# Kernel tuning notes

Measured on AMD Instinct MI355X. Metric: run time of the kernel, lower is better.

The kernel has to match this reference:

```python
import jax, jax.numpy as jnp
import numpy as np

N_AGENTS = 32
N_HEADS = 8
HEAD_DIM = 32          # atten_dim // n_heads
HID = 256              # rnn_hidden_dim
ATT = 256              # atten_dim
N_ACT = 32
NEG = -1e9             # finite stand-in for -inf; exp underflows to 0 in softmax


def setup_inputs() -> dict:
    key = jax.random.key(0)
    ks = jax.random.split(key, 20)
    B, N, E = 4096, 64, 128
    w = lambda k, shape: (jax.random.normal(k, shape, jnp.float32) * 0.05)
    return {
        "inputs": jax.random.normal(ks[0], (B, N, E), jnp.float32),
        "hidden_state": jax.random.normal(ks[1], (B, N_AGENTS, HID), jnp.float32) * 0.1,
        "fc1_w": w(ks[2], (HID, E)), "fc1_b": jnp.zeros((HID,), jnp.float32),
        "q_w": w(ks[3], (ATT, HID)), "q_b": jnp.zeros((ATT,), jnp.float32),
        "k_w": w(ks[4], (ATT, HID)), "k_b": jnp.zeros((ATT,), jnp.float32),
        "v_w": w(ks[5], (ATT, HID)), "v_b": jnp.zeros((ATT,), jnp.float32),
        "w_ih": w(ks[6], (3 * HID, ATT)), "w_hh": w(ks[7], (3 * HID, HID)),
        "b_ih": jnp.zeros((3 * HID,), jnp.float32), "b_hh": jnp.zeros((3 * HID,), jnp.float32),
        "out_w": w(ks[8], (N_ACT, HID)), "out_b": jnp.zeros((N_ACT,), jnp.float32),
        "obs_mask": jax.random.randint(ks[9], (B, N, N), 0, 2).astype(bool),
        "scenario_mask": jax.random.randint(ks[10], (B, N_AGENTS), 0, 2).astype(bool),
    }


def reference(inputs, hidden_state, fc1_w, fc1_b, q_w, q_b, k_w, k_b, v_w, v_b,
              w_ih, w_hh, b_ih, b_hh, out_w, out_b, obs_mask, scenario_mask):
    B, N, _ = inputs.shape
    A, nh, e = N_AGENTS, N_HEADS, HEAD_DIM
    # fc1 + ReLU: [B, N, HID]
    x = jax.nn.relu(inputs @ fc1_w.T + fc1_b)
    # multi-head projections; queries only for the first A entities (agents)
    q = (x[:, :A] @ q_w.T + q_b).reshape(B, A, nh, e).transpose(0, 2, 1, 3)   # [B,nh,A,e]
    k = (x @ k_w.T + k_b).reshape(B, N, nh, e).transpose(0, 2, 3, 1)          # [B,nh,e,N]
    v = jax.nn.relu(x @ v_w.T + v_b).reshape(B, N, nh, e).transpose(0, 2, 1, 3)  # [B,nh,N,e]
    score = jnp.einsum('bhae,bhen->bhan', q, k) / np.float32(np.sqrt(e))      # [B,nh,A,N]
    m = obs_mask[:, :A, :][:, None, :, :]                                      # [B,1,A,N]
    score = jnp.where(m, NEG, score)
    w = jax.nn.softmax(score, axis=-1)
    # original: fully-masked rows give NaN then are zeroed; here zero all masked slots
    w = jnp.where(m, 0.0, w)
    att = jnp.einsum('bhan,bhne->bhae', w, v)                                  # [B,nh,A,e]
    att = att.transpose(0, 2, 1, 3).reshape(B * A, nh * e)                     # [B*A, ATT]
    # GRUCell step (PyTorch gate ordering: r, z, n)
    h0 = hidden_state.reshape(B * A, HID)
    gi = att @ w_ih.T + b_ih
    gh = h0 @ w_hh.T + b_hh
    ir, iz, in_ = jnp.split(gi, 3, axis=-1)
    hr, hz, hn = jnp.split(gh, 3, axis=-1)
    r = jax.nn.sigmoid(ir + hr)
    z = jax.nn.sigmoid(iz + hz)
    n = jnp.tanh(in_ + r * hn)
    h = (1.0 - z) * n + z * h0
    h = h.reshape(B, A, HID)
    am = scenario_mask[:, :, None]                                             # [B,A,1]
    h = jnp.where(am, 0.0, h)
    q_out = h @ out_w.T + out_b
    q_out = jnp.where(am, 0.0, q_out)
    return q_out, h
```

## Files before the change

### kernel.cpp

```cpp
#include <hip/hip_runtime.h>


using bfrag = __attribute__((ext_vector_type(8))) short;
using s4    = __attribute__((ext_vector_type(4))) short;
using ffrag = __attribute__((ext_vector_type(4))) float;

#define MFMA(a,b,c) __builtin_amdgcn_mfma_f32_16x16x32_bf16((a),(b),(c),0,0,0)
#define SWZ(row,col,S,xm) ((row)*(S) + ((((col)&~7) ^ (((row)&(xm))<<3)) | ((col)&7)))

#define OFF_A2   0L
#define OFF_FC1  67108864L
#define OFF_QKV  67141632L
#define OFF_W6   67338240L
#define OFF_OW   67731456L
#define OFF_FLAG 67739648L
#define WS_NEED_BYTES 135479552L

__device__ inline unsigned short f2bf(float x){
  union { float f; unsigned u; } v; v.f = x;
  unsigned r = v.u + 0x7fffu + ((v.u >> 16) & 1u);
  return (unsigned short)(r >> 16);
}
__device__ inline bool getmask(const void* p, long i, int byteflag){
  return byteflag ? (((const unsigned char*)p)[i] != 0)
                  : (((const int*)p)[i] != 0);
}
__device__ inline ffrag fzero(){ ffrag z; z[0]=0.f; z[1]=0.f; z[2]=0.f; z[3]=0.f; return z; }
__device__ inline void gload16(const short* g, short* l){
  __builtin_amdgcn_global_load_lds((const __attribute__((address_space(1))) void*)g,
                                   (__attribute__((address_space(3))) void*)l, 16, 0, 0);
}
__device__ inline bfrag packbf(const float* p){
  float4 f0 = *(const float4*)p; float4 f1 = *(const float4*)(p+4);
  bfrag v;
  v[0]=(short)f2bf(f0.x); v[1]=(short)f2bf(f0.y); v[2]=(short)f2bf(f0.z); v[3]=(short)f2bf(f0.w);
  v[4]=(short)f2bf(f1.x); v[5]=(short)f2bf(f1.y); v[6]=(short)f2bf(f1.z); v[7]=(short)f2bf(f1.w);
  return v;
}

__global__ void k0_prep(const float* __restrict__ fc1, const float* __restrict__ qw,
    const float* __restrict__ kw, const float* __restrict__ vw, const float* __restrict__ wih,
    const float* __restrict__ whh, const float* __restrict__ ow,
    const void* __restrict__ obsm, short* __restrict__ ws){
  long tid = (long)blockIdx.x*blockDim.x + threadIdx.x;
  long n = (long)gridDim.x*blockDim.x;
  if (tid == 0){
    const int* mi = (const int*)obsm;
    int f = 0;
    for (int i=0;i<256;i++){ if ((unsigned)mi[i] > 1u){ f = 1; break; } }
    ((int*)(ws + OFF_FLAG))[0] = f;
  }
  for (long i=tid; i<32768; i+=n){
    int R = (int)(i>>7), C = (int)(i&127);
    int s = R>>6, colr = R&63, ct = colr>>4, ll = colr&15;
    int ks = C>>5, rem = C&31, lh = rem>>3, j = rem&7;
    long dst = ((long)((s*4+ks)*4+ct))*512 + (lh*16+ll)*8 + j;
    ws[OFF_FC1 + dst] = (short)f2bf(fc1[i]);
  }
  for (long i=tid; i<65536; i+=n){
    int R = (int)(i>>8), C = (int)(i&255);
    int cb = R>>6, colr = R&63, ct = colr>>4, ll = colr&15;
    int ks = C>>5, rem = C&31, lh = rem>>3, j = rem&7;
    long fo = ((long)ks)*4 + ct;
    long dst = (long)(lh*16+ll)*8 + j + fo*512;
    ws[OFF_QKV + ((long)(0*4+cb))*16384 + dst] = (short)f2bf(qw[i]);
    ws[OFF_QKV + ((long)(1*4+cb))*16384 + dst] = (short)f2bf(kw[i]);
    ws[OFF_QKV + ((long)(2*4+cb))*16384 + dst] = (short)f2bf(vw[i]);
  }
  for (long i=tid; i<196608; i+=n){
    int gate = (int)(i >> 16);
    int grow = (int)((i >> 8) & 255);
    int c = (int)(i & 255);
    int jb = grow >> 5, row = grow & 31;
    int cs = c ^ ((row&7)<<3);
    ws[OFF_W6 + ((long)((jb*6 + gate)*32 + row))*256 + cs]     = (short)f2bf(wih[i]);
    ws[OFF_W6 + ((long)((jb*6 + 3 + gate)*32 + row))*256 + cs] = (short)f2bf(whh[i]);
  }
  for (long i=tid; i<8192; i+=n) ws[OFF_OW+i] = (short)f2bf(ow[i]);
}

__global__ __launch_bounds__(512) void k1_fused(const float* __restrict__ inp,
    const short* __restrict__ fc1F, const float* __restrict__ fc1_b,
    const short* __restrict__ qkvF,
    const float* __restrict__ qb, const float* __restrict__ kb, const float* __restrict__ vb,
    const void* __restrict__ obsm, short* __restrict__ A2, const int* __restrict__ flagp){
  __shared__ __align__(16) short smem[59392];
  short* x_s  = smem;
  short* a_s  = smem + 16384;
  short* q_s  = smem + 16384;
  short* k_s  = smem + 24576;
  short* vT_s = smem + 40960;
  unsigned char* m8 = (unsigned char*)(smem + 57344);
  int t = threadIdx.x; int b = blockIdx.x;
  int lane = t&63, w = t>>6, lr = lane&15, ko = lane>>4;
  int mflag = *flagp;
  #pragma unroll
  for (int i=0;i<2;i++){
    int c = t + i*512; int row = c>>4; int cc = (c&15)*8;
    *(bfrag*)(a_s + SWZ(row, cc, 128, 7)) = packbf(inp + ((long)b*64 + row)*128 + cc);
  }
  if (mflag){
    uchar4 mv = *(const uchar4*)((const unsigned char*)obsm + (long)b*4096 + t*4);
    m8[t*4]=mv.x; m8[t*4+1]=mv.y; m8[t*4+2]=mv.z; m8[t*4+3]=mv.w;
  } else {
    int4 mv = *(const int4*)((const int*)obsm + (long)b*4096 + t*4);
    m8[t*4]  =(unsigned char)(mv.x!=0); m8[t*4+1]=(unsigned char)(mv.y!=0);
    m8[t*4+2]=(unsigned char)(mv.z!=0); m8[t*4+3]=(unsigned char)(mv.w!=0);
  }
  __syncthreads();
  {
    int rg1 = w&3, ch1 = w>>2;
    bfrag a1[4];
    #pragma unroll
    for (int ks=0;ks<4;ks++)
      a1[ks] = *(const bfrag*)(a_s + SWZ(rg1*16+lr, ks*32+ko*8, 128, 7));
    #pragma unroll
    for (int s=0;s<4;s++){
      ffrag acc[2]; acc[0]=fzero(); acc[1]=fzero();
      #pragma unroll
      for (int ks=0;ks<4;ks++){
        #pragma unroll
        for (int nt=0;nt<2;nt++){
          int ct = ch1*2 + nt;
          bfrag bb = *(const bfrag*)(fc1F + ((long)((s*4+ks)*4+ct))*512 + lane*8);
          acc[nt] = MFMA(a1[ks], bb, acc[nt]);
        }
      }
      #pragma unroll
      for (int nt=0;nt<2;nt++){
        int colg = s*64 + ch1*32 + nt*16 + lr;
        float bias = fc1_b[colg];
        #pragma unroll
        for (int r=0;r<4;r++){
          int row = rg1*16 + ko*4 + r;
          float v = acc[nt][r] + bias; v = v>0.f?v:0.f;
          x_s[SWZ(row, colg, 256, 7)] = (short)f2bf(v);
        }
      }
    }
  }
  __syncthreads();
  {
    int rg = w&1, chs = w>>1;
    bfrag a_r[2][8];
    #pragma unroll
    for (int mt=0;mt<2;mt++)
      #pragma unroll
      for (int kk=0;kk<8;kk++)
        a_r[mt][kk] = *(const bfrag*)(x_s + SWZ(rg*32+mt*16+lr, kk*32+ko*8, 256, 7));
    __syncthreads();
    for (int s=0; s<12; s++){
      int kind = s>>2, cb = s&3;
      bool active = !(kind==0 && rg==1);
      if (active){
        const short* fb = qkvF + (long)s*16384 + (long)chs*512 + lane*8;
        ffrag acc0=fzero(), acc1=fzero();
        #pragma unroll
        for (int ks=0;ks<8;ks++){
          bfrag bb = *(const bfrag*)(fb + (long)ks*2048);
          acc0 = MFMA(a_r[0][ks], bb, acc0);
          acc1 = MFMA(a_r[1][ks], bb, acc1);
        }
        int colg = cb*64 + chs*16 + lr;
        if (kind==0){
          float bias = qb[colg];
          #pragma unroll
          for (int r=0;r<4;r++){
            q_s[SWZ(ko*4+r, colg, 256, 7)]    = (short)f2bf(acc0[r] + bias);
            q_s[SWZ(16+ko*4+r, colg, 256, 7)] = (short)f2bf(acc1[r] + bias);
          }
        } else if (kind==1){
          float bias = kb[colg];
          #pragma unroll
          for (int r=0;r<4;r++){
            k_s[SWZ(rg*32+ko*4+r, colg, 256, 7)]    = (short)f2bf(acc0[r] + bias);
            k_s[SWZ(rg*32+16+ko*4+r, colg, 256, 7)] = (short)f2bf(acc1[r] + bias);
          }
        } else {
          float bias = vb[colg];
          int hh = colg>>5, e = colg&31;
          #pragma unroll
          for (int mt=0;mt<2;mt++){
            int n0 = rg*32 + mt*16 + ko*4;
            s4 pk;
            #pragma unroll
            for (int r=0;r<4;r++){
              float v = (mt?acc1[r]:acc0[r]) + bias; v = v>0.f?v:0.f;
              pk[r] = (short)f2bf(v);
            }
            *(s4*)(vT_s + hh*2048 + SWZ(e, n0, 64, 7)) = pk;
          }
        }
      }
    }
  }
  __syncthreads();
  {
    const int h = w;
    short* p_s = x_s + h*2048;
    bfrag a_q[2];
    #pragma unroll
    for (int mt=0; mt<2; mt++)
      a_q[mt] = *(const bfrag*)(q_s + SWZ(mt*16+lr, h*32+ko*8, 256, 7));
    bfrag b_k[4];
    #pragma unroll
    for (int nt=0; nt<4; nt++)
      b_k[nt] = *(const bfrag*)(k_s + SWZ(nt*16+lr, h*32+ko*8, 256, 7));
    ffrag sc[2][4];
    #pragma unroll
    for (int mt=0; mt<2; mt++)
      #pragma unroll
      for (int nt=0; nt<4; nt++) sc[mt][nt] = MFMA(a_q[mt], b_k[nt], fzero());
    const float scale = 0.17677669529663687f;
    float rsi[2][4];
    #pragma unroll
    for (int mt=0; mt<2; mt++){
      #pragma unroll
      for (int r=0; r<4; r++){
        int arow = mt*16 + ko*4 + r;
        float sv[4]; int mk[4];
        #pragma unroll
        for (int nt=0; nt<4; nt++){
          mk[nt] = m8[arow*64 + nt*16 + lr];
          sv[nt] = sc[mt][nt][r] * scale;
        }
        float mx = -3.0e38f;
        #pragma unroll
        for (int nt=0; nt<4; nt++) if (!mk[nt]) mx = fmaxf(mx, sv[nt]);
        for (int d=1; d<16; d<<=1) mx = fmaxf(mx, __shfl_xor(mx, d));
        float sum = 0.f;
        #pragma unroll
        for (int nt=0; nt<4; nt++){
          float p = mk[nt] ? 0.f : __expf(sv[nt]-mx);
          sv[nt] = p; sum += p;
        }
        for (int d=1; d<16; d<<=1) sum += __shfl_xor(sum, d);
        rsi[mt][r] = sum > 0.f ? 1.f/sum : 0.f;
        #pragma unroll
        for (int nt=0; nt<4; nt++)
          p_s[SWZ(arow, nt*16+lr, 64, 7)] = (short)f2bf(sv[nt]);
      }
    }
    ffrag o[2][2];
    #pragma unroll
    for (int mt=0;mt<2;mt++)
      #pragma unroll
      for (int nt=0;nt<2;nt++) o[mt][nt]=fzero();
    #pragma unroll
    for (int kk=0; kk<2; kk++){
      int kc = kk*32 + ko*8;
      bfrag pa0 = *(const bfrag*)(p_s + SWZ(lr,    kc, 64, 7));
      bfrag pa1 = *(const bfrag*)(p_s + SWZ(16+lr, kc, 64, 7));
      bfrag bv0 = *(const bfrag*)(vT_s + h*2048 + SWZ(lr,    kc, 64, 7));
      bfrag bv1 = *(const bfrag*)(vT_s + h*2048 + SWZ(16+lr, kc, 64, 7));
      o[0][0]=MFMA(pa0,bv0,o[0][0]); o[0][1]=MFMA(pa0,bv1,o[0][1]);
      o[1][0]=MFMA(pa1,bv0,o[1][0]); o[1][1]=MFMA(pa1,bv1,o[1][1]);
    }
    #pragma unroll
    for (int mt=0; mt<2; mt++)
      #pragma unroll
      for (int nt=0; nt<2; nt++)
        #pragma unroll
        for (int r=0; r<4; r++){
          int a = mt*16 + ko*4 + r;
          A2[((long)b*32 + a)*256 + h*32 + nt*16 + lr] = (short)f2bf(o[mt][nt][r]*rsi[mt][r]);
        }
  }
}

__global__ __launch_bounds__(512) void k3_gru(const short* __restrict__ A2,
    const float* __restrict__ h0f, const short* __restrict__ w6,
    const float* __restrict__ b_ih, const float* __restrict__ b_hh,
    const void* __restrict__ scen, float* __restrict__ hout, const int* __restrict__ flagp){
  __shared__ __align__(16) short w_s[2][16384];
  int t = threadIdx.x, bid = blockIdx.x;
  long R0 = (long)bid * 128;
  int mflag = *flagp;
  int lane = t&63, w = t>>6, lr = lane&15, ko = lane>>4;
  long rowbase = R0 + (long)w*16;
  auto STAGE = [&](int ph){
    const short* src = w6 + (long)ph*16384;
    short* dst = w_s[ph&1];
    #pragma unroll
    for (int i=0;i<4;i++)
      gload16(src + (long)(i*512 + t)*8, dst + (i*512 + (t & ~63))*8);
  };
  STAGE(0);
  const short* Ab = A2 + (rowbase + lr)*256 + ko*8;
  const float* Hb = h0f + (rowbase + lr)*256 + ko*8;
  bfrag A[16];
  #pragma unroll
  for (int ks=0; ks<8; ks++)
    A[ks] = *(const bfrag*)(Ab + ks*32);
  #pragma unroll
  for (int ks=0; ks<8; ks++)
    A[8+ks] = packbf(Hb + ks*32);
  __syncthreads();
  for (int jb=0; jb<8; jb++){
    ffrag aR[2], aZ[2], aI[2], aN[2];
    #pragma unroll
    for (int nt=0;nt<2;nt++){ aR[nt]=fzero(); aZ[nt]=fzero(); aI[nt]=fzero(); aN[nt]=fzero(); }
    #pragma unroll
    for (int p=0; p<3; p++){
      int ph = jb*3 + p;
      if (ph < 23) STAGE(ph+1);
      const short* wc = w_s[ph&1];
      #pragma unroll
      for (int ks=0; ks<8; ks++){
        int kc = ks*32 + ko*8;
        #pragma unroll
        for (int nt=0; nt<2; nt++){
          bfrag b0 = *(const bfrag*)(wc + SWZ(nt*16+lr, kc, 256, 7));
          bfrag b1 = *(const bfrag*)(wc + 8192 + SWZ(nt*16+lr, kc, 256, 7));
          if (p == 0){
            aR[nt] = MFMA(A[ks], b0, aR[nt]);
            aZ[nt] = MFMA(A[ks], b1, aZ[nt]);
          } else if (p == 1){
            aI[nt] = MFMA(A[ks], b0, aI[nt]);
            aR[nt] = MFMA(A[8+ks], b1, aR[nt]);
          } else {
            aZ[nt] = MFMA(A[8+ks], b0, aZ[nt]);
            aN[nt] = MFMA(A[8+ks], b1, aN[nt]);
          }
        }
      }
      if (p == 2){
        #pragma unroll
        for (int nt=0; nt<2; nt++){
          int j = jb*32 + nt*16 + lr;
          float bir = b_ih[j],     bhr = b_hh[j];
          float biz = b_ih[256+j], bhz = b_hh[256+j];
          float bin = b_ih[512+j], bhn = b_hh[512+j];
          #pragma unroll
          for (int rr=0; rr<4; rr++){
            long row = rowbase + ko*4 + rr;
            float rg = 1.f/(1.f + __expf(-(aR[nt][rr] + bir + bhr)));
            float zg = 1.f/(1.f + __expf(-(aZ[nt][rr] + biz + bhz)));
            float ag = aI[nt][rr] + bin + rg*(aN[nt][rr] + bhn);
            float ng = 2.f/(1.f + __expf(-2.f*ag)) - 1.f;
            float h0v = h0f[row*256 + j];
            float hv = (1.f - zg)*ng + zg*h0v;
            if (getmask(scen, row, mflag)) hv = 0.f;
            hout[row*256 + j] = hv;
          }
        }
      }
      __syncthreads();
    }
  }
}

__global__ __launch_bounds__(512) void k4_out(const float* __restrict__ hout,
    const short* __restrict__ ow, const float* __restrict__ out_b,
    const void* __restrict__ scen, float* __restrict__ qout, const int* __restrict__ flagp){
  __shared__ __align__(16) short ow_s[32*256];
  int t = threadIdx.x; long R0 = (long)blockIdx.x * 256;
  int mflag = *flagp;
  for (int i=0;i<2;i++){
    int c = t + i*512; int row = c >> 5; int cc = (c & 31)*8;
    *(bfrag*)(ow_s + SWZ(row, cc, 256, 7)) = *(const bfrag*)(ow + row*256 + cc);
  }
  __syncthreads();
  int lane = t&63, w = t>>6, lr = lane&15, ko = lane>>4;
  ffrag acc[2][2];
  #pragma unroll
  for (int a=0;a<2;a++) for (int bq=0;bq<2;bq++) acc[a][bq]=fzero();
  for (int ks=0; ks<8; ks++){
    int kc = ks*32 + ko*8;
    #pragma unroll
    for (int mi=0; mi<2; mi++){
      long row = R0 + (w*2+mi)*16 + lr;
      bfrag a = packbf(hout + row*256 + kc);
      #pragma unroll
      for (int nt=0; nt<2; nt++){
        bfrag bb = *(const bfrag*)(ow_s + SWZ(nt*16+lr, kc, 256, 7));
        acc[mi][nt] = MFMA(a, bb, acc[mi][nt]);
      }
    }
  }
  #pragma unroll
  for (int mi=0;mi<2;mi++)
    #pragma unroll
    for (int nt=0;nt<2;nt++){
      int col = nt*16 + lr;
      float ob = out_b[col];
      #pragma unroll
      for (int r=0;r<4;r++){
        long row = R0 + (w*2+mi)*16 + ko*4 + r;
        float qv = acc[mi][nt][r] + ob;
        if (getmask(scen, row, mflag)) qv = 0.f;
        qout[row*32 + col] = qv;
      }
    }
}

extern "C" void kernel_launch(void* const* d_in, const int* in_sizes, int n_in,
                              void* d_out, int out_size, void* d_ws, size_t ws_size,
                              hipStream_t stream){
  const float* inputs = (const float*)d_in[0];
  const float* hidden = (const float*)d_in[1];
  const float* fc1_w  = (const float*)d_in[2];
  const float* fc1_b  = (const float*)d_in[3];
  const float* q_w    = (const float*)d_in[4];
  const float* q_b    = (const float*)d_in[5];
  const float* k_w    = (const float*)d_in[6];
  const float* k_b    = (const float*)d_in[7];
  const float* v_w    = (const float*)d_in[8];
  const float* v_b    = (const float*)d_in[9];
  const float* w_ih   = (const float*)d_in[10];
  const float* w_hh   = (const float*)d_in[11];
  const float* b_ih   = (const float*)d_in[12];
  const float* b_hh   = (const float*)d_in[13];
  const float* out_w  = (const float*)d_in[14];
  const float* out_b  = (const float*)d_in[15];
  const void* obsm    = d_in[16];
  const void* scen    = d_in[17];
  (void)in_sizes; (void)n_in; (void)out_size;
  if ((long)ws_size < WS_NEED_BYTES) return;
  short* ws = (short*)d_ws;
  const int* flagp = (const int*)(ws + OFF_FLAG);
  float* qout = (float*)d_out;
  float* hout = qout + 4194304;
  short* A2  = ws + OFF_A2;

  hipLaunchKernelGGL(k0_prep, dim3(512), dim3(256), 0, stream,
      fc1_w, q_w, k_w, v_w, w_ih, w_hh, out_w, obsm, ws);
  hipLaunchKernelGGL(k1_fused, dim3(4096), dim3(512), 0, stream,
      inputs, ws + OFF_FC1, fc1_b, ws + OFF_QKV, q_b, k_b, v_b, obsm, A2, flagp);
  hipLaunchKernelGGL(k3_gru, dim3(1024), dim3(512), 0, stream,
      A2, hidden, ws + OFF_W6, b_ih, b_hh, scen, hout, flagp);
  hipLaunchKernelGGL(k4_out, dim3(512), dim3(512), 0, stream,
      hout, ws + OFF_OW, out_b, scen, qout, flagp);
}
```

Measured before the change: 532.6 us.

## Split QKV projection and attention into two head-group passes to shrink LDS

The fused k1 kernel now computes the Q/K/V projections and attention in two passes of four heads each instead of all eight at once. This halves the q/k/vT shared-memory staging, cutting LDS per block from about 116KB to about 76KB so more blocks can be resident per CU. In exchange, only half the waves do attention work in each pass, and extra barriers are added per pass. The x_s buffer is kept live across both passes, since its A operands stay in registers and p_s reuses x_s.

```diff
diff --git a/kernel.cpp b/kernel.cpp
--- a/kernel.cpp
+++ b/kernel.cpp
@@ -84,13 +84,13 @@
     const short* __restrict__ qkvF,
     const float* __restrict__ qb, const float* __restrict__ kb, const float* __restrict__ vb,
     const void* __restrict__ obsm, short* __restrict__ A2, const int* __restrict__ flagp){
-  __shared__ __align__(16) short smem[59392];
+  __shared__ __align__(16) short smem[38912];
   short* x_s  = smem;
-  short* a_s  = smem + 16384;
   short* q_s  = smem + 16384;
-  short* k_s  = smem + 24576;
-  short* vT_s = smem + 40960;
-  unsigned char* m8 = (unsigned char*)(smem + 57344);
+  short* k_s  = smem + 20480;
+  short* a_s  = smem + 20480;
+  short* vT_s = smem + 28672;
+  unsigned char* m8 = (unsigned char*)(smem + 36864);
   int t = threadIdx.x; int b = blockIdx.x;
   int lane = t&63, w = t>>6, lr = lane&15, ko = lane>>4;
   int mflag = *flagp;
@@ -140,17 +140,19 @@
     }
   }
   __syncthreads();
-  {
-    int rg = w&1, chs = w>>1;
-    bfrag a_r[2][8];
-    #pragma unroll
-    for (int mt=0;mt<2;mt++)
-      #pragma unroll
-      for (int kk=0;kk<8;kk++)
-        a_r[mt][kk] = *(const bfrag*)(x_s + SWZ(rg*32+mt*16+lr, kk*32+ko*8, 256, 7));
-    __syncthreads();
-    for (int s=0; s<12; s++){
-      int kind = s>>2, cb = s&3;
+  int rg = w&1, chs = w>>1;
+  bfrag a_r[2][8];
+  #pragma unroll
+  for (int mt=0;mt<2;mt++)
+    #pragma unroll
+    for (int kk=0;kk<8;kk++)
+      a_r[mt][kk] = *(const bfrag*)(x_s + SWZ(rg*32+mt*16+lr, kk*32+ko*8, 256, 7));
+  for (int hg=0; hg<2; hg++){
+    #pragma unroll
+    for (int s6=0; s6<6; s6++){
+      int kind = s6>>1, cbl = s6&1;
+      int cb = hg*2 + cbl;
+      int s = kind*4 + cb;
       bool active = !(kind==0 && rg==1);
       if (active){
         const short* fb = qkvF + (long)s*16384 + (long)chs*512 + lane*8;
@@ -162,23 +164,24 @@
           acc1 = MFMA(a_r[1][ks], bb, acc1);
         }
         int colg = cb*64 + chs*16 + lr;
+        int cl = cbl*64 + chs*16 + lr;
         if (kind==0){
           float bias = qb[colg];
           #pragma unroll
           for (int r=0;r<4;r++){
-            q_s[SWZ(ko*4+r, colg, 256, 7)]    = (short)f2bf(acc0[r] + bias);
-            q_s[SWZ(16+ko*4+r, colg, 256, 7)] = (short)f2bf(acc1[r] + bias);
+            q_s[SWZ(ko*4+r, cl, 128, 7)]    = (short)f2bf(acc0[r] + bias);
+            q_s[SWZ(16+ko*4+r, cl, 128, 7)] = (short)f2bf(acc1[r] + bias);
           }
         } else if (kind==1){
           float bias = kb[colg];
           #pragma unroll
           for (int r=0;r<4;r++){
-            k_s[SWZ(rg*32+ko*4+r, colg, 256, 7)]    = (short)f2bf(acc0[r] + bias);
-            k_s[SWZ(rg*32+16+ko*4+r, colg, 256, 7)] = (short)f2bf(acc1[r] + bias);
+            k_s[SWZ(rg*32+ko*4+r, cl, 128, 7)]    = (short)f2bf(acc0[r] + bias);
+            k_s[SWZ(rg*32+16+ko*4+r, cl, 128, 7)] = (short)f2bf(acc1[r] + bias);
           }
         } else {
           float bias = vb[colg];
-          int hh = colg>>5, e = colg&31;
+          int hh = cl>>5, e = cl&31;
           #pragma unroll
           for (int mt=0;mt<2;mt++){
             int n0 = rg*32 + mt*16 + ko*4;
@@ -193,78 +196,79 @@
         }
       }
     }
-  }
-  __syncthreads();
-  {
-    const int h = w;
-    short* p_s = x_s + h*2048;
-    bfrag a_q[2];
-    #pragma unroll
-    for (int mt=0; mt<2; mt++)
-      a_q[mt] = *(const bfrag*)(q_s + SWZ(mt*16+lr, h*32+ko*8, 256, 7));
-    bfrag b_k[4];
-    #pragma unroll
-    for (int nt=0; nt<4; nt++)
-      b_k[nt] = *(const bfrag*)(k_s + SWZ(nt*16+lr, h*32+ko*8, 256, 7));
-    ffrag sc[2][4];
-    #pragma unroll
-    for (int mt=0; mt<2; mt++)
-      #pragma unroll
-      for (int nt=0; nt<4; nt++) sc[mt][nt] = MFMA(a_q[mt], b_k[nt], fzero());
-    const float scale = 0.17677669529663687f;
-    float rsi[2][4];
-    #pragma unroll
-    for (int mt=0; mt<2; mt++){
-      #pragma unroll
-      for (int r=0; r<4; r++){
-        int arow = mt*16 + ko*4 + r;
-        float sv[4]; int mk[4];
-        #pragma unroll
-        for (int nt=0; nt<4; nt++){
-          mk[nt] = m8[arow*64 + nt*16 + lr];
-          sv[nt] = sc[mt][nt][r] * scale;
-        }
-        float mx = -3.0e38f;
-        #pragma unroll
-        for (int nt=0; nt<4; nt++) if (!mk[nt]) mx = fmaxf(mx, sv[nt]);
-        for (int d=1; d<16; d<<=1) mx = fmaxf(mx, __shfl_xor(mx, d));
-        float sum = 0.f;
-        #pragma unroll
-        for (int nt=0; nt<4; nt++){
-          float p = mk[nt] ? 0.f : __expf(sv[nt]-mx);
-          sv[nt] = p; sum += p;
-        }
-        for (int d=1; d<16; d<<=1) sum += __shfl_xor(sum, d);
-        rsi[mt][r] = sum > 0.f ? 1.f/sum : 0.f;
-        #pragma unroll
-        for (int nt=0; nt<4; nt++)
-          p_s[SWZ(arow, nt*16+lr, 64, 7)] = (short)f2bf(sv[nt]);
-      }
-    }
-    ffrag o[2][2];
-    #pragma unroll
-    for (int mt=0;mt<2;mt++)
-      #pragma unroll
-      for (int nt=0;nt<2;nt++) o[mt][nt]=fzero();
-    #pragma unroll
-    for (int kk=0; kk<2; kk++){
-      int kc = kk*32 + ko*8;
-      bfrag pa0 = *(const bfrag*)(p_s + SWZ(lr,    kc, 64, 7));
-      bfrag pa1 = *(const bfrag*)(p_s + SWZ(16+lr, kc, 64, 7));
-      bfrag bv0 = *(const bfrag*)(vT_s + h*2048 + SWZ(lr,    kc, 64, 7));
-      bfrag bv1 = *(const bfrag*)(vT_s + h*2048 + SWZ(16+lr, kc, 64, 7));
-      o[0][0]=MFMA(pa0,bv0,o[0][0]); o[0][1]=MFMA(pa0,bv1,o[0][1]);
-      o[1][0]=MFMA(pa1,bv0,o[1][0]); o[1][1]=MFMA(pa1,bv1,o[1][1]);
-    }
-    #pragma unroll
-    for (int mt=0; mt<2; mt++)
-      #pragma unroll
-      for (int nt=0; nt<2; nt++)
+    __syncthreads();
+    if (w < 4){
+      int hloc = w, h = hg*4 + w;
+      short* p_s = x_s + hloc*2048;
+      bfrag a_q[2];
+      #pragma unroll
+      for (int mt=0; mt<2; mt++)
+        a_q[mt] = *(const bfrag*)(q_s + SWZ(mt*16+lr, hloc*32+ko*8, 128, 7));
+      bfrag b_k[4];
+      #pragma unroll
+      for (int nt=0; nt<4; nt++)
+        b_k[nt] = *(const bfrag*)(k_s + SWZ(nt*16+lr, hloc*32+ko*8, 128, 7));
+      ffrag sc[2][4];
+      #pragma unroll
+      for (int mt=0; mt<2; mt++)
+        #pragma unroll
+        for (int nt=0; nt<4; nt++) sc[mt][nt] = MFMA(a_q[mt], b_k[nt], fzero());
+      const float scale = 0.17677669529663687f;
+      float rsi[2][4];
+      #pragma unroll
+      for (int mt=0; mt<2; mt++){
         #pragma unroll
         for (int r=0; r<4; r++){
-          int a = mt*16 + ko*4 + r;
-          A2[((long)b*32 + a)*256 + h*32 + nt*16 + lr] = (short)f2bf(o[mt][nt][r]*rsi[mt][r]);
-        }
+          int arow = mt*16 + ko*4 + r;
+          float sv[4]; int mk[4];
+          #pragma unroll
+          for (int nt=0; nt<4; nt++){
+            mk[nt] = m8[arow*64 + nt*16 + lr];
+            sv[nt] = sc[mt][nt][r] * scale;
+          }
+          float mx = -3.0e38f;
+          #pragma unroll
+          for (int nt=0; nt<4; nt++) if (!mk[nt]) mx = fmaxf(mx, sv[nt]);
+          for (int d=1; d<16; d<<=1) mx = fmaxf(mx, __shfl_xor(mx, d));
+          float sum = 0.f;
+          #pragma unroll
+          for (int nt=0; nt<4; nt++){
+            float p = mk[nt] ? 0.f : __expf(sv[nt]-mx);
+            sv[nt] = p; sum += p;
+          }
+          for (int d=1; d<16; d<<=1) sum += __shfl_xor(sum, d);
+          rsi[mt][r] = sum > 0.f ? 1.f/sum : 0.f;
+          #pragma unroll
+          for (int nt=0; nt<4; nt++)
+            p_s[SWZ(arow, nt*16+lr, 64, 7)] = (short)f2bf(sv[nt]);
+        }
+      }
+      ffrag o[2][2];
+      #pragma unroll
+      for (int mt=0;mt<2;mt++)
+        #pragma unroll
+        for (int nt=0;nt<2;nt++) o[mt][nt]=fzero();
+      #pragma unroll
+      for (int kk=0; kk<2; kk++){
+        int kc = kk*32 + ko*8;
+        bfrag pa0 = *(const bfrag*)(p_s + SWZ(lr,    kc, 64, 7));
+        bfrag pa1 = *(const bfrag*)(p_s + SWZ(16+lr, kc, 64, 7));
+        bfrag bv0 = *(const bfrag*)(vT_s + hloc*2048 + SWZ(lr,    kc, 64, 7));
+        bfrag bv1 = *(const bfrag*)(vT_s + hloc*2048 + SWZ(16+lr, kc, 64, 7));
+        o[0][0]=MFMA(pa0,bv0,o[0][0]); o[0][1]=MFMA(pa0,bv1,o[0][1]);
+        o[1][0]=MFMA(pa1,bv0,o[1][0]); o[1][1]=MFMA(pa1,bv1,o[1][1]);
+      }
+      #pragma unroll
+      for (int mt=0; mt<2; mt++)
+        #pragma unroll
+        for (int nt=0; nt<2; nt++)
+          #pragma unroll
+          for (int r=0; r<4; r++){
+            int a = mt*16 + ko*4 + r;
+            A2[((long)b*32 + a)*256 + h*32 + nt*16 + lr] = (short)f2bf(o[mt][nt][r]*rsi[mt][r]);
+          }
+    }
+    __syncthreads();
   }
 }
 
```

After: 587.8 us. 1.1x slower.

## Fuse output projection into GRU kernel via shared-memory staged hidden state

Applied to the files above, without the earlier changes.

Removes the separate output-projection kernel. The GRU kernel now writes each bf16 hidden row into a new 64KB shared buffer and then computes q_out with MFMA, using output weights pre-packed in fragment order. This avoids one launch and re-reading the full fp32 hidden output from global memory. The extra shared memory (w_s plus h_s, 128KB) may reduce occupancy of the GRU kernel. It also adds full unrolling of the QKV projection loop in k1.

```diff
diff --git a/kernel.cpp b/kernel.cpp
--- a/kernel.cpp
+++ b/kernel.cpp
@@ -76,7 +76,13 @@
     ws[OFF_W6 + ((long)((jb*6 + gate)*32 + row))*256 + cs]     = (short)f2bf(wih[i]);
     ws[OFF_W6 + ((long)((jb*6 + 3 + gate)*32 + row))*256 + cs] = (short)f2bf(whh[i]);
   }
-  for (long i=tid; i<8192; i+=n) ws[OFF_OW+i] = (short)f2bf(ow[i]);
+  for (long i=tid; i<8192; i+=n){
+    int R = (int)(i>>8), C = (int)(i&255);
+    int nt = R>>4, ll = R&15;
+    int ks = C>>5, rem = C&31, lh = rem>>3, j = rem&7;
+    long dst = ((long)(ks*2+nt))*512 + (lh*16+ll)*8 + j;
+    ws[OFF_OW + dst] = (short)f2bf(ow[i]);
+  }
 }
 
 __global__ __launch_bounds__(512) void k1_fused(const float* __restrict__ inp,
@@ -149,6 +155,7 @@
       for (int kk=0;kk<8;kk++)
         a_r[mt][kk] = *(const bfrag*)(x_s + SWZ(rg*32+mt*16+lr, kk*32+ko*8, 256, 7));
     __syncthreads();
+    #pragma unroll
     for (int s=0; s<12; s++){
       int kind = s>>2, cb = s&3;
       bool active = !(kind==0 && rg==1);
@@ -271,8 +278,11 @@
 __global__ __launch_bounds__(512) void k3_gru(const short* __restrict__ A2,
     const float* __restrict__ h0f, const short* __restrict__ w6,
     const float* __restrict__ b_ih, const float* __restrict__ b_hh,
-    const void* __restrict__ scen, float* __restrict__ hout, const int* __restrict__ flagp){
+    const short* __restrict__ owF, const float* __restrict__ out_b,
+    const void* __restrict__ scen, float* __restrict__ hout, float* __restrict__ qout,
+    const int* __restrict__ flagp){
   __shared__ __align__(16) short w_s[2][16384];
+  __shared__ __align__(16) short h_s[32768];
   int t = threadIdx.x, bid = blockIdx.x;
   long R0 = (long)bid * 128;
   int mflag = *flagp;
@@ -333,7 +343,8 @@
           float bin = b_ih[512+j], bhn = b_hh[512+j];
           #pragma unroll
           for (int rr=0; rr<4; rr++){
-            long row = rowbase + ko*4 + rr;
+            int rowl = w*16 + ko*4 + rr;
+            long row = R0 + rowl;
             float rg = 1.f/(1.f + __expf(-(aR[nt][rr] + bir + bhr)));
             float zg = 1.f/(1.f + __expf(-(aZ[nt][rr] + biz + bhz)));
             float ag = aI[nt][rr] + bin + rg*(aN[nt][rr] + bhn);
@@ -342,56 +353,40 @@
             float hv = (1.f - zg)*ng + zg*h0v;
             if (getmask(scen, row, mflag)) hv = 0.f;
             hout[row*256 + j] = hv;
+            h_s[SWZ(rowl, j, 256, 7)] = (short)f2bf(hv);
           }
         }
       }
       __syncthreads();
     }
   }
-}
-
-__global__ __launch_bounds__(512) void k4_out(const float* __restrict__ hout,
-    const short* __restrict__ ow, const float* __restrict__ out_b,
-    const void* __restrict__ scen, float* __restrict__ qout, const int* __restrict__ flagp){
-  __shared__ __align__(16) short ow_s[32*256];
-  int t = threadIdx.x; long R0 = (long)blockIdx.x * 256;
-  int mflag = *flagp;
-  for (int i=0;i<2;i++){
-    int c = t + i*512; int row = c >> 5; int cc = (c & 31)*8;
-    *(bfrag*)(ow_s + SWZ(row, cc, 256, 7)) = *(const bfrag*)(ow + row*256 + cc);
-  }
-  __syncthreads();
-  int lane = t&63, w = t>>6, lr = lane&15, ko = lane>>4;
-  ffrag acc[2][2];
-  #pragma unroll
-  for (int a=0;a<2;a++) for (int bq=0;bq<2;bq++) acc[a][bq]=fzero();
-  for (int ks=0; ks<8; ks++){
-    int kc = ks*32 + ko*8;
-    #pragma unroll
-    for (int mi=0; mi<2; mi++){
-      long row = R0 + (w*2+mi)*16 + lr;
-      bfrag a = packbf(hout + row*256 + kc);
+  {
+    bfrag ah[8];
+    #pragma unroll
+    for (int ks=0; ks<8; ks++)
+      ah[ks] = *(const bfrag*)(h_s + SWZ(w*16+lr, ks*32+ko*8, 256, 7));
+    ffrag oq[2]; oq[0]=fzero(); oq[1]=fzero();
+    #pragma unroll
+    for (int ks=0; ks<8; ks++){
       #pragma unroll
       for (int nt=0; nt<2; nt++){
-        bfrag bb = *(const bfrag*)(ow_s + SWZ(nt*16+lr, kc, 256, 7));
-        acc[mi][nt] = MFMA(a, bb, acc[mi][nt]);
-      }
-    }
-  }
-  #pragma unroll
-  for (int mi=0;mi<2;mi++)
-    #pragma unroll
-    for (int nt=0;nt<2;nt++){
+        bfrag bb = *(const bfrag*)(owF + ((long)(ks*2+nt))*512 + lane*8);
+        oq[nt] = MFMA(ah[ks], bb, oq[nt]);
+      }
+    }
+    #pragma unroll
+    for (int nt=0; nt<2; nt++){
       int col = nt*16 + lr;
       float ob = out_b[col];
       #pragma unroll
       for (int r=0;r<4;r++){
-        long row = R0 + (w*2+mi)*16 + ko*4 + r;
-        float qv = acc[mi][nt][r] + ob;
+        long row = rowbase + ko*4 + r;
+        float qv = oq[nt][r] + ob;
         if (getmask(scen, row, mflag)) qv = 0.f;
         qout[row*32 + col] = qv;
       }
     }
+  }
 }
 
 extern "C" void kernel_launch(void* const* d_in, const int* in_sizes, int n_in,
@@ -428,7 +423,5 @@
   hipLaunchKernelGGL(k1_fused, dim3(4096), dim3(512), 0, stream,
       inputs, ws + OFF_FC1, fc1_b, ws + OFF_QKV, q_b, k_b, v_b, obsm, A2, flagp);
   hipLaunchKernelGGL(k3_gru, dim3(1024), dim3(512), 0, stream,
-      A2, hidden, ws + OFF_W6, b_ih, b_hh, scen, hout, flagp);
-  hipLaunchKernelGGL(k4_out, dim3(512), dim3(512), 0, stream,
-      hout, ws + OFF_OW, out_b, scen, qout, flagp);
-}
+      A2, hidden, ws + OFF_W6, b_ih, b_hh, ws + OFF_OW, out_b, scen, hout, qout, flagp);
+}
```

New measurement: 530.9 us. No clear change (-0.3%).
